# Optimization experiments

Hardware: AMD Instinct MI355X
Metric: run time of the kernel (lower is better)

The kernel has to match this reference:

```python
import jax, jax.numpy as jnp
import numpy as np

B, C, H, W = 8, 512, 96, 96
CQ = C // 4


def setup_inputs() -> dict:
    key = jax.random.key(0)
    ks = jax.random.split(key, 8)
    s = 1.0 / np.sqrt(C)
    return {
        "x": jax.random.normal(ks[0], (B, C, H, W), jnp.float32),
        "Wq": jax.random.normal(ks[1], (CQ, C), jnp.float32) * s,
        "bq": jax.random.normal(ks[2], (CQ,), jnp.float32) * 0.01,
        "Wk": jax.random.normal(ks[3], (CQ, C), jnp.float32) * s,
        "bk": jax.random.normal(ks[4], (CQ,), jnp.float32) * 0.01,
        "Wv": jax.random.normal(ks[5], (C, C), jnp.float32) * s,
        "bv": jax.random.normal(ks[6], (C,), jnp.float32) * 0.01,
        "gamma": jax.random.normal(ks[7], (1,), jnp.float32) * 0.1,
    }


def _conv1x1(x, Wt, b):
    # 1x1 conv == per-pixel channel matmul: [B,C,H,W] x [O,C] -> [B,O,H,W]
    return jnp.einsum("bchw,oc->bohw", x, Wt) + b[None, :, None, None]


def reference(x, Wq, bq, Wk, bk, Wv, bv, gamma):
    b, c, h, w = x.shape
    q = _conv1x1(x, Wq, bq)  # [B,CQ,H,W]
    k = _conv1x1(x, Wk, bk)  # [B,CQ,H,W]
    v = _conv1x1(x, Wv, bv)  # [B,C ,H,W]

    # column (height-axis) attention energies, diagonal masked to -inf
    energy_H = jnp.einsum("bchw,bcjw->bhwj", q, k)  # [B,H,W,H]
    diag = jnp.eye(h, dtype=bool)[:, None, :]  # [H,1,H] broadcast over W
    energy_H = jnp.where(diag[None], -jnp.inf, energy_H)
    # row (width-axis) attention energies
    energy_W = jnp.einsum("bchw,bchj->bhwj", q, k)  # [B,H,W,W]

    att = jax.nn.softmax(jnp.concatenate([energy_H, energy_W], axis=3), axis=3)
    att_H = att[..., :h]       # [B,H,W,H]
    att_W = att[..., h:h + w]  # [B,H,W,W]

    out_H = jnp.einsum("bcjw,bhwj->bchw", v, att_H)
    out_W = jnp.einsum("bchj,bhwj->bchw", v, att_W)
    return gamma[0] * (out_H + out_W) + x
```

## Files before the change

### kernel.cpp

```cpp
#include <hip/hip_runtime.h>


#define B_ 8
#define C_ 512
#define CQ_ 128
#define H_ 96
#define W_ 96
#define HW_ 9216
#define J_ 192

typedef __attribute__((ext_vector_type(8))) short short8;
typedef __attribute__((ext_vector_type(4))) float f32x4;

__device__ __forceinline__ unsigned short f2bf(float f) {
    unsigned u = __float_as_uint(f);
    u += 0x7FFFu + ((u >> 16) & 1u);
    return (unsigned short)(u >> 16);
}
__device__ __forceinline__ float bf2f(unsigned short h) {
    return __uint_as_float((unsigned)h << 16);
}
__device__ __forceinline__ unsigned short f2h(float f) {
    _Float16 h = (_Float16)f;
    return __builtin_bit_cast(unsigned short, h);
}
__device__ __forceinline__ float h2f(unsigned short u) {
    return (float)__builtin_bit_cast(_Float16, u);
}
__device__ __forceinline__ void gl_lds16(const unsigned short* g, void* lds_base) {
    __builtin_amdgcn_global_load_lds((const __attribute__((address_space(1))) void*)g,
                                     (__attribute__((address_space(3))) void*)lds_base,
                                     16, 0, 0);
}

__global__ __launch_bounds__(256) void k0_wconv(const float* __restrict__ Wq,
                                                const float* __restrict__ Wk,
                                                const float* __restrict__ Wv,
                                                unsigned short* __restrict__ Wqk,
                                                unsigned short* __restrict__ Wvb) {
    int i = blockIdx.x * 256 + threadIdx.x;
    if (i < 65536)        Wqk[i] = f2bf(Wq[i]);
    else if (i < 131072)  Wqk[i] = f2bf(Wk[i - 65536]);
    else                  Wvb[i - 131072] = f2bf(Wv[i - 131072]);
}

__global__ __launch_bounds__(256) void k1_xT(const float* __restrict__ x,
                                             unsigned short* __restrict__ xT) {
    __shared__ unsigned short t[32][33];
    int b = blockIdx.z, c0 = blockIdx.y * 32, p0 = blockIdx.x * 32;
    int tx = threadIdx.x, ty = threadIdx.y;
    const float* xb = x + (size_t)b * C_ * HW_;
    #pragma unroll
    for (int k = 0; k < 4; ++k) {
        int c = c0 + ty + k * 8;
        t[ty + k * 8][tx] = f2bf(xb[(size_t)c * HW_ + p0 + tx]);
    }
    __syncthreads();
    unsigned short* xTb = xT + (size_t)b * HW_ * C_;
    #pragma unroll
    for (int k = 0; k < 4; ++k) {
        int p = p0 + ty + k * 8;
        xTb[(size_t)p * C_ + c0 + tx] = t[tx][ty + k * 8];
    }
}

__global__ __launch_bounds__(512) void k2a_qk(const unsigned short* __restrict__ xT,
                                              const unsigned short* __restrict__ Wqk,
                                              const float* __restrict__ bq,
                                              const float* __restrict__ bk,
                                              unsigned short* __restrict__ Qb,
                                              unsigned short* __restrict__ Kb) {
    __shared__ alignas(16) unsigned short As[128][64];
    __shared__ alignas(16) unsigned short Bs[256][64];
    int t = threadIdx.x;
    int p0 = blockIdx.x * 128;
    int wid = t >> 6, lane = t & 63;
    int wr = wid >> 2, wc = wid & 3;
    int srow = lane >> 3, sk8 = (lane & 7) << 3;
    const f32x4 zero = {0.f, 0.f, 0.f, 0.f};
    f32x4 acc[4][4];
    for (int m = 0; m < 4; ++m) for (int n = 0; n < 4; ++n) acc[m][n] = zero;
    for (int ks = 0; ks < 512; ks += 64) {
        #pragma unroll
        for (int i = 0; i < 2; ++i) {
            int q = wid * 2 + i; int row = q * 8 + srow;
            gl_lds16(xT + ((size_t)(p0 + row) << 9) + ks + sk8, (char*)&As[0][0] + q * 1024);
        }
        #pragma unroll
        for (int i = 0; i < 4; ++i) {
            int q = wid * 4 + i; int row = q * 8 + srow;
            gl_lds16(Wqk + ((size_t)row << 9) + ks + sk8, (char*)&Bs[0][0] + q * 1024);
        }
        __syncthreads();
        #pragma unroll
        for (int kk = 0; kk < 2; ++kk) {
            int ko = (kk << 5) + ((lane >> 4) << 3);
            short8 af[4], bfv[4];
            #pragma unroll
            for (int m = 0; m < 4; ++m) af[m] = *(const short8*)(&As[wr * 64 + m * 16 + (lane & 15)][ko]);
            #pragma unroll
            for (int n = 0; n < 4; ++n) bfv[n] = *(const short8*)(&Bs[wc * 64 + n * 16 + (lane & 15)][ko]);
            #pragma unroll
            for (int m = 0; m < 4; ++m)
                #pragma unroll
                for (int n = 0; n < 4; ++n)
                    acc[m][n] = __builtin_amdgcn_mfma_f32_16x16x32_bf16(af[m], bfv[n], acc[m][n], 0, 0, 0);
        }
        __syncthreads();
    }
    #pragma unroll
    for (int n = 0; n < 4; ++n) {
        int oc = wc * 64 + n * 16 + (lane & 15);
        float bias = (oc < 128) ? bq[oc] : bk[oc - 128];
        unsigned short* dst = (oc < 128) ? (Qb + oc) : (Kb + (oc - 128));
        #pragma unroll
        for (int m = 0; m < 4; ++m) {
            int pr = p0 + wr * 64 + m * 16 + ((lane >> 4) << 2);
            #pragma unroll
            for (int r = 0; r < 4; ++r)
                dst[(size_t)(pr + r) << 7] = f2bf(acc[m][n][r] + bias);
        }
    }
}

__global__ __launch_bounds__(512) void k2b_v(const unsigned short* __restrict__ xT,
                                             const unsigned short* __restrict__ Wvb,
                                             const float* __restrict__ bv,
                                             unsigned short* __restrict__ Vn) {
    __shared__ alignas(16) unsigned short As[512][64];
    __shared__ alignas(16) unsigned short Bs[64][64];
    int t = threadIdx.x;
    int p0 = blockIdx.x * 64;
    int wid = t >> 6, lane = t & 63;
    int wr = wid >> 1, wc = wid & 1;
    int srow = lane >> 3, sk8 = (lane & 7) << 3;
    const f32x4 zero = {0.f, 0.f, 0.f, 0.f};
    f32x4 acc[8][2];
    for (int m = 0; m < 8; ++m) for (int n = 0; n < 2; ++n) acc[m][n] = zero;
    for (int ks = 0; ks < 512; ks += 64) {
        #pragma unroll
        for (int i = 0; i < 8; ++i) {
            int q = wid * 8 + i; int row = q * 8 + srow;
            gl_lds16(Wvb + ((size_t)row << 9) + ks + sk8, (char*)&As[0][0] + q * 1024);
        }
        {
            int q = wid; int row = q * 8 + srow;
            gl_lds16(xT + ((size_t)(p0 + row) << 9) + ks + sk8, (char*)&Bs[0][0] + q * 1024);
        }
        __syncthreads();
        #pragma unroll
        for (int kk = 0; kk < 2; ++kk) {
            int ko = (kk << 5) + ((lane >> 4) << 3);
            short8 af[8], bfv[2];
            #pragma unroll
            for (int m = 0; m < 8; ++m) af[m] = *(const short8*)(&As[wr * 128 + m * 16 + (lane & 15)][ko]);
            #pragma unroll
            for (int n = 0; n < 2; ++n) bfv[n] = *(const short8*)(&Bs[wc * 32 + n * 16 + (lane & 15)][ko]);
            #pragma unroll
            for (int m = 0; m < 8; ++m)
                #pragma unroll
                for (int n = 0; n < 2; ++n)
                    acc[m][n] = __builtin_amdgcn_mfma_f32_16x16x32_bf16(af[m], bfv[n], acc[m][n], 0, 0, 0);
        }
        __syncthreads();
    }
    int b = p0 / HW_;
    int hw0 = p0 - b * HW_;
    #pragma unroll
    for (int m = 0; m < 8; ++m) {
        int ocb = wr * 128 + m * 16 + ((lane >> 4) << 2);
        #pragma unroll
        for (int n = 0; n < 2; ++n) {
            int hw = hw0 + wc * 32 + n * 16 + (lane & 15);
            #pragma unroll
            for (int r = 0; r < 4; ++r) {
                int oc = ocb + r;
                Vn[(size_t)(b * C_ + oc) * HW_ + hw] = f2bf(acc[m][n][r] + bv[oc]);
            }
        }
    }
}

__global__ __launch_bounds__(256) void k3_vt(const unsigned short* __restrict__ Vn,
                                             unsigned short* __restrict__ Vt) {
    __shared__ unsigned short tl[96][97];
    int plane = blockIdx.x;
    const unsigned short* src = Vn + (size_t)plane * HW_;
    unsigned short* dst = Vt + (size_t)plane * HW_;
    for (int e = threadIdx.x; e < HW_; e += 256) tl[e / 96][e % 96] = src[e];
    __syncthreads();
    for (int e = threadIdx.x; e < HW_; e += 256) { int w = e / 96, h = e % 96; dst[e] = tl[h][w]; }
}

__global__ __launch_bounds__(256) void k4_energy(const unsigned short* __restrict__ Qb,
                                                 const unsigned short* __restrict__ Kb,
                                                 unsigned short* __restrict__ att) {
    __shared__ alignas(16) unsigned short Qs[96][136];
    __shared__ alignas(16) unsigned short Ks[96][136];
    int t = threadIdx.x;
    int modeH = blockIdx.z;
    int b = blockIdx.y, v0 = blockIdx.x;
    size_t base, rstride, obase_off, ostride;
    if (!modeH) {
        base      = (size_t)((b * H_ + v0) * W_) * CQ_;
        rstride   = CQ_;
        obase_off = (size_t)((b * H_ + v0) * W_) * J_ + H_;
        ostride   = J_;
    } else {
        base      = ((size_t)(b * H_) * W_ + v0) * CQ_;
        rstride   = (size_t)W_ * CQ_;
        obase_off = ((size_t)(b * H_) * W_ + v0) * J_;
        ostride   = (size_t)W_ * J_;
    }
    for (int q = t; q < 1536; q += 256) {
        int row = q >> 4, c8 = (q & 15) << 3;
        *(uint4*)(&Qs[row][c8]) = *(const uint4*)(Qb + base + (size_t)row * rstride + c8);
        *(uint4*)(&Ks[row][c8]) = *(const uint4*)(Kb + base + (size_t)row * rstride + c8);
    }
    __syncthreads();
    int wid = t >> 6, lane = t & 63;
    int wr = wid >> 1, wc = wid & 1;
    const f32x4 zero = {0.f, 0.f, 0.f, 0.f};
    f32x4 acc[3][3];
    for (int m = 0; m < 3; ++m) for (int n = 0; n < 3; ++n) acc[m][n] = zero;
    #pragma unroll
    for (int ks = 0; ks < 128; ks += 32) {
        int ko = ks + ((lane >> 4) << 3);
        short8 af[3], bfv[3];
        #pragma unroll
        for (int m = 0; m < 3; ++m) af[m] = *(const short8*)(&Qs[wr * 48 + m * 16 + (lane & 15)][ko]);
        #pragma unroll
        for (int n = 0; n < 3; ++n) bfv[n] = *(const short8*)(&Ks[wc * 48 + n * 16 + (lane & 15)][ko]);
        #pragma unroll
        for (int m = 0; m < 3; ++m)
            #pragma unroll
            for (int n = 0; n < 3; ++n)
                acc[m][n] = __builtin_amdgcn_mfma_f32_16x16x32_bf16(af[m], bfv[n], acc[m][n], 0, 0, 0);
    }
    unsigned short* ob = att + obase_off;
    #pragma unroll
    for (int m = 0; m < 3; ++m) {
        int i = wr * 48 + m * 16 + ((lane >> 4) << 2);
        #pragma unroll
        for (int n = 0; n < 3; ++n) {
            int j = wc * 48 + n * 16 + (lane & 15);
            #pragma unroll
            for (int r = 0; r < 4; ++r) {
                float v = acc[m][n][r];
                if (modeH && (i + r) == j) v = -__builtin_inff();
                ob[(size_t)(i + r) * ostride + j] = f2h(v);
            }
        }
    }
}

__global__ __launch_bounds__(256) void k5_softmax(const unsigned short* __restrict__ att,
                                                  unsigned short* __restrict__ att2) {
    int r = blockIdx.x * 4 + (threadIdx.x >> 6);
    int lane = threadIdx.x & 63;
    const unsigned short* row = att + (size_t)r * J_;
    float e0 = h2f(row[lane]), e1 = h2f(row[lane + 64]), e2 = h2f(row[lane + 128]);
    float m = fmaxf(e0, fmaxf(e1, e2));
    #pragma unroll
    for (int off = 32; off; off >>= 1) m = fmaxf(m, __shfl_xor(m, off, 64));
    float p0 = __expf(e0 - m), p1 = __expf(e1 - m), p2 = __expf(e2 - m);
    float s = p0 + p1 + p2;
    #pragma unroll
    for (int off = 32; off; off >>= 1) s += __shfl_xor(s, off, 64);
    float inv = 1.f / s;
    unsigned short* orow = att2 + (size_t)r * J_;
    orow[lane]       = f2bf(p0 * inv);
    orow[lane + 64]  = f2bf(p1 * inv);
    orow[lane + 128] = f2bf(p2 * inv);
}

template <int MODE>
__global__ __launch_bounds__(256) void k67_agg(const unsigned short* __restrict__ Vsrc,
                                               const unsigned short* __restrict__ att2,
                                               unsigned short* __restrict__ dst) {
    __shared__ alignas(16) unsigned short As[128][104];
    __shared__ alignas(16) unsigned short Bs[96][104];
    int t = threadIdx.x;
    int c0 = blockIdx.x * 128;
    int b = blockIdx.y / 96;
    int v0 = blockIdx.y % 96;
    size_t abase, bbase, bstride;
    if (MODE == 0) {
        abase = (size_t)(b * C_ + c0) * HW_ + (size_t)v0 * W_;
        bbase = (size_t)((b * H_ + v0) * W_) * J_ + H_;
        bstride = J_;
    } else {
        abase = ((size_t)(b * C_ + c0) * W_ + v0) * H_;
        bbase = ((size_t)(b * H_) * W_ + v0) * J_;
        bstride = (size_t)W_ * J_;
    }
    {
        int row = t >> 1, cs = (t & 1) * 6;
        const unsigned short* src = Vsrc + abase + (size_t)row * HW_;
        #pragma unroll
        for (int i = 0; i < 6; ++i)
            *(uint4*)(&As[row][(cs + i) * 8]) = *(const uint4*)(src + (cs + i) * 8);
    }
    if (t < 192) {
        int row = t >> 1, cs = (t & 1) * 6;
        const unsigned short* src = att2 + bbase + (size_t)row * bstride;
        #pragma unroll
        for (int i = 0; i < 6; ++i)
            *(uint4*)(&Bs[row][(cs + i) * 8]) = *(const uint4*)(src + (cs + i) * 8);
    }
    __syncthreads();
    int wid = t >> 6, lane = t & 63;
    const f32x4 zero = {0.f, 0.f, 0.f, 0.f};
    f32x4 acc[2][6];
    for (int m = 0; m < 2; ++m) for (int n = 0; n < 6; ++n) acc[m][n] = zero;
    #pragma unroll
    for (int ks = 0; ks < 96; ks += 32) {
        int ko = ks + ((lane >> 4) << 3);
        short8 af[2], bfv[6];
        #pragma unroll
        for (int m = 0; m < 2; ++m) af[m] = *(const short8*)(&As[wid * 32 + m * 16 + (lane & 15)][ko]);
        #pragma unroll
        for (int n = 0; n < 6; ++n) bfv[n] = *(const short8*)(&Bs[n * 16 + (lane & 15)][ko]);
        #pragma unroll
        for (int m = 0; m < 2; ++m)
            #pragma unroll
            for (int n = 0; n < 6; ++n)
                acc[m][n] = __builtin_amdgcn_mfma_f32_16x16x32_bf16(af[m], bfv[n], acc[m][n], 0, 0, 0);
    }
    #pragma unroll
    for (int m = 0; m < 2; ++m) {
        int crel = wid * 32 + m * 16 + ((lane >> 4) << 2);
        #pragma unroll
        for (int n = 0; n < 6; ++n) {
            int col = n * 16 + (lane & 15);
            #pragma unroll
            for (int r = 0; r < 4; ++r)
                dst[abase + (size_t)(crel + r) * HW_ + col] = f2bf(acc[m][n][r]);
        }
    }
}

__global__ __launch_bounds__(256) void k8b_combine(const unsigned short* __restrict__ tmpW,
                                                   const unsigned short* __restrict__ tmpHT,
                                                   const float* __restrict__ x,
                                                   const float* __restrict__ gamma_p,
                                                   float* __restrict__ outp) {
    __shared__ unsigned tlp[96][49];
    int plane = blockIdx.x;
    int t = threadIdx.x;
    const unsigned short* src = tmpHT + (size_t)plane * HW_;
    for (int e = t; e < 1152; e += 256) {
        int w = e / 12, h8 = (e % 12) * 8;
        uint4 v = *(const uint4*)(src + w * 96 + h8);
        tlp[w][(h8 >> 1) + 0] = v.x;
        tlp[w][(h8 >> 1) + 1] = v.y;
        tlp[w][(h8 >> 1) + 2] = v.z;
        tlp[w][(h8 >> 1) + 3] = v.w;
    }
    __syncthreads();
    float g = gamma_p[0];
    const unsigned short* wp = tmpW + (size_t)plane * HW_;
    const float* xp = x + (size_t)plane * HW_;
    float* op = outp + (size_t)plane * HW_;
    #pragma unroll
    for (int i = 0; i < 9; ++i) {
        int m = t + 256 * i;
        int h = m / 24, w0 = (m % 24) * 4;
        int off = h * 96 + w0;
        f32x4 xv = *(const f32x4*)(xp + off);
        uint2 tw = *(const uint2*)(wp + off);
        unsigned short ws0 = (unsigned short)(tw.x & 0xFFFF);
        unsigned short ws1 = (unsigned short)(tw.x >> 16);
        unsigned short ws2 = (unsigned short)(tw.y & 0xFFFF);
        unsigned short ws3 = (unsigned short)(tw.y >> 16);
        f32x4 o;
        #pragma unroll
        for (int r = 0; r < 4; ++r) {
            unsigned u = tlp[w0 + r][h >> 1];
            unsigned short hv = (h & 1) ? (unsigned short)(u >> 16) : (unsigned short)(u & 0xFFFF);
            unsigned short wv = (r == 0) ? ws0 : (r == 1) ? ws1 : (r == 2) ? ws2 : ws3;
            o[r] = g * (bf2f(wv) + bf2f(hv)) + xv[r];
        }
        *(f32x4*)(op + off) = o;
    }
}

extern "C" void kernel_launch(void* const* d_in, const int* in_sizes, int n_in,
                              void* d_out, int out_size, void* d_ws, size_t ws_size,
                              hipStream_t stream) {
    const float* x  = (const float*)d_in[0];
    const float* Wq = (const float*)d_in[1];
    const float* bq = (const float*)d_in[2];
    const float* Wk = (const float*)d_in[3];
    const float* bk = (const float*)d_in[4];
    const float* Wv = (const float*)d_in[5];
    const float* bv = (const float*)d_in[6];
    const float* gm = (const float*)d_in[7];
    float* out = (float*)d_out;
    char* ws = (char*)d_ws;

    unsigned short* xT    = (unsigned short*)(ws + 0);
    unsigned short* attf  = (unsigned short*)(ws + 0);
    unsigned short* Vt    = (unsigned short*)(ws + 0);
    unsigned short* Vn    = (unsigned short*)(ws + 75497472);
    unsigned short* Qb    = (unsigned short*)(ws + 150994944);
    unsigned short* Kb    = (unsigned short*)(ws + 169869312);
    unsigned short* att2  = (unsigned short*)(ws + 150994944);
    unsigned short* Wqk   = (unsigned short*)(ws + 188743680);
    unsigned short* Wvb   = (unsigned short*)(ws + 189005824);

    k0_wconv<<<1536, 256, 0, stream>>>(Wq, Wk, Wv, Wqk, Wvb);
    k1_xT<<<dim3(288, 16, 8), dim3(32, 8, 1), 0, stream>>>(x, xT);
    k2a_qk<<<576, 512, 0, stream>>>(xT, Wqk, bq, bk, Qb, Kb);
    k2b_v<<<1152, 512, 0, stream>>>(xT, Wvb, bv, Vn);
    k4_energy<<<dim3(96, 8, 2), 256, 0, stream>>>(Qb, Kb, attf);
    k5_softmax<<<18432, 256, 0, stream>>>(attf, att2);
    k3_vt<<<4096, 256, 0, stream>>>(Vn, Vt);
    k67_agg<0><<<dim3(4, 768), 256, 0, stream>>>(Vn, att2, Vn);
    k67_agg<1><<<dim3(4, 768), 256, 0, stream>>>(Vt, att2, Vt);
    k8b_combine<<<4096, 256, 0, stream>>>(Vn, Vt, x, gm, out);
}
```

Measured before the change: 379.0 us.

## Aggregate attention over x first, then apply the V projection with fused epilogue

Uses linearity of the 1x1 value conv to aggregate bf16 x with the attention weights first and apply Wv plus bias afterwards, since the attention rows sum to one. The projection GEMM's epilogue applies gamma and the residual directly, which removes the separate V GEMM output, the V transpose and the combine kernel. x is staged as bf16 planes and their transposes in the output buffer as scratch. The shared-memory tiles of the QK and projection GEMMs get an XOR swizzle to reduce bank conflicts. The risk is bf16 rounding of the summed aggregate across the two aggregation passes, and reuse of the output buffer as scratch.

```diff
diff --git a/kernel.cpp b/kernel.cpp
--- a/kernel.cpp
+++ b/kernel.cpp
@@ -45,7 +45,8 @@
 }
 
 __global__ __launch_bounds__(256) void k1_xT(const float* __restrict__ x,
-                                             unsigned short* __restrict__ xT) {
+                                             unsigned short* __restrict__ xT,
+                                             unsigned short* __restrict__ xP) {
     __shared__ unsigned short t[32][33];
     int b = blockIdx.z, c0 = blockIdx.y * 32, p0 = blockIdx.x * 32;
     int tx = threadIdx.x, ty = threadIdx.y;
@@ -53,7 +54,9 @@
     #pragma unroll
     for (int k = 0; k < 4; ++k) {
         int c = c0 + ty + k * 8;
-        t[ty + k * 8][tx] = f2bf(xb[(size_t)c * HW_ + p0 + tx]);
+        unsigned short v = f2bf(xb[(size_t)c * HW_ + p0 + tx]);
+        t[ty + k * 8][tx] = v;
+        xP[((size_t)b * C_ + c) * HW_ + p0 + tx] = v;
     }
     __syncthreads();
     unsigned short* xTb = xT + (size_t)b * HW_ * C_;
@@ -62,6 +65,17 @@
         int p = p0 + ty + k * 8;
         xTb[(size_t)p * C_ + c0 + tx] = t[tx][ty + k * 8];
     }
+}
+
+__global__ __launch_bounds__(256) void k3_vt(const unsigned short* __restrict__ src_,
+                                             unsigned short* __restrict__ dst_) {
+    __shared__ unsigned short tl[96][97];
+    int plane = blockIdx.x;
+    const unsigned short* src = src_ + (size_t)plane * HW_;
+    unsigned short* dst = dst_ + (size_t)plane * HW_;
+    for (int e = threadIdx.x; e < HW_; e += 256) tl[e / 96][e % 96] = src[e];
+    __syncthreads();
+    for (int e = threadIdx.x; e < HW_; e += 256) { int w = e / 96, h = e % 96; dst[e] = tl[h][w]; }
 }
 
 __global__ __launch_bounds__(512) void k2a_qk(const unsigned short* __restrict__ xT,
@@ -76,7 +90,8 @@
     int p0 = blockIdx.x * 128;
     int wid = t >> 6, lane = t & 63;
     int wr = wid >> 2, wc = wid & 3;
-    int srow = lane >> 3, sk8 = (lane & 7) << 3;
+    int srow = lane >> 3;
+    int sk8 = (((lane & 7) ^ srow) << 3);
     const f32x4 zero = {0.f, 0.f, 0.f, 0.f};
     f32x4 acc[4][4];
     for (int m = 0; m < 4; ++m) for (int n = 0; n < 4; ++n) acc[m][n] = zero;
@@ -94,12 +109,12 @@
         __syncthreads();
         #pragma unroll
         for (int kk = 0; kk < 2; ++kk) {
-            int ko = (kk << 5) + ((lane >> 4) << 3);
+            int po = (((kk * 4 + (lane >> 4)) ^ (lane & 7)) << 3);
             short8 af[4], bfv[4];
             #pragma unroll
-            for (int m = 0; m < 4; ++m) af[m] = *(const short8*)(&As[wr * 64 + m * 16 + (lane & 15)][ko]);
-            #pragma unroll
-            for (int n = 0; n < 4; ++n) bfv[n] = *(const short8*)(&Bs[wc * 64 + n * 16 + (lane & 15)][ko]);
+            for (int m = 0; m < 4; ++m) af[m] = *(const short8*)(&As[wr * 64 + m * 16 + (lane & 15)][po]);
+            #pragma unroll
+            for (int n = 0; n < 4; ++n) bfv[n] = *(const short8*)(&Bs[wc * 64 + n * 16 + (lane & 15)][po]);
             #pragma unroll
             for (int m = 0; m < 4; ++m)
                 #pragma unroll
@@ -121,75 +136,6 @@
                 dst[(size_t)(pr + r) << 7] = f2bf(acc[m][n][r] + bias);
         }
     }
-}
-
-__global__ __launch_bounds__(512) void k2b_v(const unsigned short* __restrict__ xT,
-                                             const unsigned short* __restrict__ Wvb,
-                                             const float* __restrict__ bv,
-                                             unsigned short* __restrict__ Vn) {
-    __shared__ alignas(16) unsigned short As[512][64];
-    __shared__ alignas(16) unsigned short Bs[64][64];
-    int t = threadIdx.x;
-    int p0 = blockIdx.x * 64;
-    int wid = t >> 6, lane = t & 63;
-    int wr = wid >> 1, wc = wid & 1;
-    int srow = lane >> 3, sk8 = (lane & 7) << 3;
-    const f32x4 zero = {0.f, 0.f, 0.f, 0.f};
-    f32x4 acc[8][2];
-    for (int m = 0; m < 8; ++m) for (int n = 0; n < 2; ++n) acc[m][n] = zero;
-    for (int ks = 0; ks < 512; ks += 64) {
-        #pragma unroll
-        for (int i = 0; i < 8; ++i) {
-            int q = wid * 8 + i; int row = q * 8 + srow;
-            gl_lds16(Wvb + ((size_t)row << 9) + ks + sk8, (char*)&As[0][0] + q * 1024);
-        }
-        {
-            int q = wid; int row = q * 8 + srow;
-            gl_lds16(xT + ((size_t)(p0 + row) << 9) + ks + sk8, (char*)&Bs[0][0] + q * 1024);
-        }
-        __syncthreads();
-        #pragma unroll
-        for (int kk = 0; kk < 2; ++kk) {
-            int ko = (kk << 5) + ((lane >> 4) << 3);
-            short8 af[8], bfv[2];
-            #pragma unroll
-            for (int m = 0; m < 8; ++m) af[m] = *(const short8*)(&As[wr * 128 + m * 16 + (lane & 15)][ko]);
-            #pragma unroll
-            for (int n = 0; n < 2; ++n) bfv[n] = *(const short8*)(&Bs[wc * 32 + n * 16 + (lane & 15)][ko]);
-            #pragma unroll
-            for (int m = 0; m < 8; ++m)
-                #pragma unroll
-                for (int n = 0; n < 2; ++n)
-                    acc[m][n] = __builtin_amdgcn_mfma_f32_16x16x32_bf16(af[m], bfv[n], acc[m][n], 0, 0, 0);
-        }
-        __syncthreads();
-    }
-    int b = p0 / HW_;
-    int hw0 = p0 - b * HW_;
-    #pragma unroll
-    for (int m = 0; m < 8; ++m) {
-        int ocb = wr * 128 + m * 16 + ((lane >> 4) << 2);
-        #pragma unroll
-        for (int n = 0; n < 2; ++n) {
-            int hw = hw0 + wc * 32 + n * 16 + (lane & 15);
-            #pragma unroll
-            for (int r = 0; r < 4; ++r) {
-                int oc = ocb + r;
-                Vn[(size_t)(b * C_ + oc) * HW_ + hw] = f2bf(acc[m][n][r] + bv[oc]);
-            }
-        }
-    }
-}
-
-__global__ __launch_bounds__(256) void k3_vt(const unsigned short* __restrict__ Vn,
-                                             unsigned short* __restrict__ Vt) {
-    __shared__ unsigned short tl[96][97];
-    int plane = blockIdx.x;
-    const unsigned short* src = Vn + (size_t)plane * HW_;
-    unsigned short* dst = Vt + (size_t)plane * HW_;
-    for (int e = threadIdx.x; e < HW_; e += 256) tl[e / 96][e % 96] = src[e];
-    __syncthreads();
-    for (int e = threadIdx.x; e < HW_; e += 256) { int w = e / 96, h = e % 96; dst[e] = tl[h][w]; }
 }
 
 __global__ __launch_bounds__(256) void k4_energy(const unsigned short* __restrict__ Qb,
@@ -275,113 +221,129 @@
 }
 
 template <int MODE>
-__global__ __launch_bounds__(256) void k67_agg(const unsigned short* __restrict__ Vsrc,
-                                               const unsigned short* __restrict__ att2,
-                                               unsigned short* __restrict__ dst) {
-    __shared__ alignas(16) unsigned short As[128][104];
-    __shared__ alignas(16) unsigned short Bs[96][104];
+__global__ __launch_bounds__(512) void k6_agg(const unsigned short* __restrict__ att2,
+                                              const unsigned short* __restrict__ Xsrc,
+                                              unsigned short* __restrict__ xAgg) {
+    __shared__ alignas(16) unsigned short As[96][104];
+    __shared__ alignas(16) unsigned short Bs[256][104];
     int t = threadIdx.x;
-    int c0 = blockIdx.x * 128;
+    int c0 = blockIdx.x * 256;
     int b = blockIdx.y / 96;
-    int v0 = blockIdx.y % 96;
-    size_t abase, bbase, bstride;
-    if (MODE == 0) {
-        abase = (size_t)(b * C_ + c0) * HW_ + (size_t)v0 * W_;
-        bbase = (size_t)((b * H_ + v0) * W_) * J_ + H_;
-        bstride = J_;
-    } else {
-        abase = ((size_t)(b * C_ + c0) * W_ + v0) * H_;
-        bbase = ((size_t)(b * H_) * W_ + v0) * J_;
-        bstride = (size_t)W_ * J_;
+    int v = blockIdx.y % 96;
+    size_t abase, astride;
+    if (MODE == 0) { abase = ((size_t)(b * HW_) + (size_t)v * 96) * J_ + 96; astride = J_; }
+    else           { abase = (size_t)(b * HW_) * J_ + (size_t)v * J_;        astride = (size_t)96 * J_; }
+    if (t < 192) {
+        int row = t >> 1, cs = (t & 1) * 6;
+        const unsigned short* src = att2 + abase + (size_t)row * astride;
+        #pragma unroll
+        for (int i = 0; i < 6; ++i)
+            *(uint4*)(&As[row][(cs + i) * 8]) = *(const uint4*)(src + (cs + i) * 8);
     }
     {
         int row = t >> 1, cs = (t & 1) * 6;
-        const unsigned short* src = Vsrc + abase + (size_t)row * HW_;
-        #pragma unroll
-        for (int i = 0; i < 6; ++i)
-            *(uint4*)(&As[row][(cs + i) * 8]) = *(const uint4*)(src + (cs + i) * 8);
-    }
-    if (t < 192) {
-        int row = t >> 1, cs = (t & 1) * 6;
-        const unsigned short* src = att2 + bbase + (size_t)row * bstride;
+        const unsigned short* src = Xsrc + ((size_t)(b * C_) + c0 + row) * HW_ + v * 96;
         #pragma unroll
         for (int i = 0; i < 6; ++i)
             *(uint4*)(&Bs[row][(cs + i) * 8]) = *(const uint4*)(src + (cs + i) * 8);
     }
     __syncthreads();
     int wid = t >> 6, lane = t & 63;
+    int wr = wid >> 2, wc = wid & 3;
     const f32x4 zero = {0.f, 0.f, 0.f, 0.f};
-    f32x4 acc[2][6];
-    for (int m = 0; m < 2; ++m) for (int n = 0; n < 6; ++n) acc[m][n] = zero;
+    f32x4 acc[3][4];
+    for (int m = 0; m < 3; ++m) for (int n = 0; n < 4; ++n) acc[m][n] = zero;
     #pragma unroll
     for (int ks = 0; ks < 96; ks += 32) {
         int ko = ks + ((lane >> 4) << 3);
-        short8 af[2], bfv[6];
-        #pragma unroll
-        for (int m = 0; m < 2; ++m) af[m] = *(const short8*)(&As[wid * 32 + m * 16 + (lane & 15)][ko]);
-        #pragma unroll
-        for (int n = 0; n < 6; ++n) bfv[n] = *(const short8*)(&Bs[n * 16 + (lane & 15)][ko]);
-        #pragma unroll
-        for (int m = 0; m < 2; ++m)
-            #pragma unroll
-            for (int n = 0; n < 6; ++n)
+        short8 af[3], bfv[4];
+        #pragma unroll
+        for (int m = 0; m < 3; ++m) af[m] = *(const short8*)(&As[wr * 48 + m * 16 + (lane & 15)][ko]);
+        #pragma unroll
+        for (int n = 0; n < 4; ++n) bfv[n] = *(const short8*)(&Bs[wc * 64 + n * 16 + (lane & 15)][ko]);
+        #pragma unroll
+        for (int m = 0; m < 3; ++m)
+            #pragma unroll
+            for (int n = 0; n < 4; ++n)
                 acc[m][n] = __builtin_amdgcn_mfma_f32_16x16x32_bf16(af[m], bfv[n], acc[m][n], 0, 0, 0);
     }
     #pragma unroll
-    for (int m = 0; m < 2; ++m) {
-        int crel = wid * 32 + m * 16 + ((lane >> 4) << 2);
-        #pragma unroll
-        for (int n = 0; n < 6; ++n) {
-            int col = n * 16 + (lane & 15);
-            #pragma unroll
-            for (int r = 0; r < 4; ++r)
-                dst[abase + (size_t)(crel + r) * HW_ + col] = f2bf(acc[m][n][r]);
-        }
-    }
-}
-
-__global__ __launch_bounds__(256) void k8b_combine(const unsigned short* __restrict__ tmpW,
-                                                   const unsigned short* __restrict__ tmpHT,
-                                                   const float* __restrict__ x,
-                                                   const float* __restrict__ gamma_p,
-                                                   float* __restrict__ outp) {
-    __shared__ unsigned tlp[96][49];
-    int plane = blockIdx.x;
+    for (int m = 0; m < 3; ++m) {
+        int orow = wr * 48 + m * 16 + ((lane >> 4) << 2);
+        #pragma unroll
+        for (int n = 0; n < 4; ++n) {
+            int c = c0 + wc * 64 + n * 16 + (lane & 15);
+            #pragma unroll
+            for (int r = 0; r < 4; ++r) {
+                int p = (MODE == 0) ? (v * 96 + orow + r) : ((orow + r) * 96 + v);
+                size_t o = ((size_t)(b * HW_) + p) * C_ + c;
+                if (MODE == 0) xAgg[o] = f2bf(acc[m][n][r]);
+                else           xAgg[o] = f2bf(bf2f(xAgg[o]) + acc[m][n][r]);
+            }
+        }
+    }
+}
+
+__global__ __launch_bounds__(512) void k9_proj(const unsigned short* __restrict__ xAgg,
+                                               const unsigned short* __restrict__ Wvb,
+                                               const float* __restrict__ bv,
+                                               const float* __restrict__ x,
+                                               const float* __restrict__ gamma_p,
+                                               float* __restrict__ outp) {
+    __shared__ alignas(16) unsigned short As[512][64];
+    __shared__ alignas(16) unsigned short Bs[64][64];
     int t = threadIdx.x;
-    const unsigned short* src = tmpHT + (size_t)plane * HW_;
-    for (int e = t; e < 1152; e += 256) {
-        int w = e / 12, h8 = (e % 12) * 8;
-        uint4 v = *(const uint4*)(src + w * 96 + h8);
-        tlp[w][(h8 >> 1) + 0] = v.x;
-        tlp[w][(h8 >> 1) + 1] = v.y;
-        tlp[w][(h8 >> 1) + 2] = v.z;
-        tlp[w][(h8 >> 1) + 3] = v.w;
-    }
-    __syncthreads();
+    int p0 = blockIdx.x * 64;
+    int wid = t >> 6, lane = t & 63;
+    int wr = wid >> 1, wc = wid & 1;
+    int srow = lane >> 3;
+    int sk8 = (((lane & 7) ^ srow) << 3);
+    const f32x4 zero = {0.f, 0.f, 0.f, 0.f};
+    f32x4 acc[8][2];
+    for (int m = 0; m < 8; ++m) for (int n = 0; n < 2; ++n) acc[m][n] = zero;
+    for (int ks = 0; ks < 512; ks += 64) {
+        #pragma unroll
+        for (int i = 0; i < 8; ++i) {
+            int q = wid * 8 + i; int row = q * 8 + srow;
+            gl_lds16(Wvb + ((size_t)row << 9) + ks + sk8, (char*)&As[0][0] + q * 1024);
+        }
+        {
+            int q = wid; int row = q * 8 + srow;
+            gl_lds16(xAgg + ((size_t)(p0 + row) << 9) + ks + sk8, (char*)&Bs[0][0] + q * 1024);
+        }
+        __syncthreads();
+        #pragma unroll
+        for (int kk = 0; kk < 2; ++kk) {
+            int po = (((kk * 4 + (lane >> 4)) ^ (lane & 7)) << 3);
+            short8 af[8], bfv[2];
+            #pragma unroll
+            for (int m = 0; m < 8; ++m) af[m] = *(const short8*)(&As[wr * 128 + m * 16 + (lane & 15)][po]);
+            #pragma unroll
+            for (int n = 0; n < 2; ++n) bfv[n] = *(const short8*)(&Bs[wc * 32 + n * 16 + (lane & 15)][po]);
+            #pragma unroll
+            for (int m = 0; m < 8; ++m)
+                #pragma unroll
+                for (int n = 0; n < 2; ++n)
+                    acc[m][n] = __builtin_amdgcn_mfma_f32_16x16x32_bf16(af[m], bfv[n], acc[m][n], 0, 0, 0);
+        }
+        __syncthreads();
+    }
+    int b = blockIdx.x / 144;
+    int hw0 = (blockIdx.x % 144) * 64;
     float g = gamma_p[0];
-    const unsigned short* wp = tmpW + (size_t)plane * HW_;
-    const float* xp = x + (size_t)plane * HW_;
-    float* op = outp + (size_t)plane * HW_;
-    #pragma unroll
-    for (int i = 0; i < 9; ++i) {
-        int m = t + 256 * i;
-        int h = m / 24, w0 = (m % 24) * 4;
-        int off = h * 96 + w0;
-        f32x4 xv = *(const f32x4*)(xp + off);
-        uint2 tw = *(const uint2*)(wp + off);
-        unsigned short ws0 = (unsigned short)(tw.x & 0xFFFF);
-        unsigned short ws1 = (unsigned short)(tw.x >> 16);
-        unsigned short ws2 = (unsigned short)(tw.y & 0xFFFF);
-        unsigned short ws3 = (unsigned short)(tw.y >> 16);
-        f32x4 o;
-        #pragma unroll
-        for (int r = 0; r < 4; ++r) {
-            unsigned u = tlp[w0 + r][h >> 1];
-            unsigned short hv = (h & 1) ? (unsigned short)(u >> 16) : (unsigned short)(u & 0xFFFF);
-            unsigned short wv = (r == 0) ? ws0 : (r == 1) ? ws1 : (r == 2) ? ws2 : ws3;
-            o[r] = g * (bf2f(wv) + bf2f(hv)) + xv[r];
-        }
-        *(f32x4*)(op + off) = o;
+    #pragma unroll
+    for (int m = 0; m < 8; ++m) {
+        int ocb = wr * 128 + m * 16 + ((lane >> 4) << 2);
+        #pragma unroll
+        for (int n = 0; n < 2; ++n) {
+            int hw = hw0 + wc * 32 + n * 16 + (lane & 15);
+            #pragma unroll
+            for (int r = 0; r < 4; ++r) {
+                int oc = ocb + r;
+                size_t o = ((size_t)(b * C_ + oc)) * HW_ + hw;
+                outp[o] = g * (acc[m][n][r] + bv[oc]) + x[o];
+            }
+        }
     }
 }
 
@@ -400,23 +362,23 @@
     char* ws = (char*)d_ws;
 
     unsigned short* xT    = (unsigned short*)(ws + 0);
-    unsigned short* attf  = (unsigned short*)(ws + 0);
-    unsigned short* Vt    = (unsigned short*)(ws + 0);
-    unsigned short* Vn    = (unsigned short*)(ws + 75497472);
-    unsigned short* Qb    = (unsigned short*)(ws + 150994944);
-    unsigned short* Kb    = (unsigned short*)(ws + 169869312);
-    unsigned short* att2  = (unsigned short*)(ws + 150994944);
-    unsigned short* Wqk   = (unsigned short*)(ws + 188743680);
-    unsigned short* Wvb   = (unsigned short*)(ws + 189005824);
+    unsigned short* xAgg  = (unsigned short*)(ws + 0);
+    unsigned short* Qb    = (unsigned short*)(ws + 75497472);
+    unsigned short* Kb    = (unsigned short*)(ws + 94371840);
+    unsigned short* attf  = (unsigned short*)(ws + 113246208);
+    unsigned short* att2  = (unsigned short*)(ws + 141557760);
+    unsigned short* Wqk   = (unsigned short*)(ws + 169869312);
+    unsigned short* Wvb   = (unsigned short*)(ws + 170131456);
+    unsigned short* xP    = (unsigned short*)d_out;
+    unsigned short* xPT   = xP + 37748736;
 
     k0_wconv<<<1536, 256, 0, stream>>>(Wq, Wk, Wv, Wqk, Wvb);
-    k1_xT<<<dim3(288, 16, 8), dim3(32, 8, 1), 0, stream>>>(x, xT);
+    k1_xT<<<dim3(288, 16, 8), dim3(32, 8, 1), 0, stream>>>(x, xT, xP);
     k2a_qk<<<576, 512, 0, stream>>>(xT, Wqk, bq, bk, Qb, Kb);
-    k2b_v<<<1152, 512, 0, stream>>>(xT, Wvb, bv, Vn);
+    k3_vt<<<4096, 256, 0, stream>>>(xP, xPT);
     k4_energy<<<dim3(96, 8, 2), 256, 0, stream>>>(Qb, Kb, attf);
     k5_softmax<<<18432, 256, 0, stream>>>(attf, att2);
-    k3_vt<<<4096, 256, 0, stream>>>(Vn, Vt);
-    k67_agg<0><<<dim3(4, 768), 256, 0, stream>>>(Vn, att2, Vn);
-    k67_agg<1><<<dim3(4, 768), 256, 0, stream>>>(Vt, att2, Vt);
-    k8b_combine<<<4096, 256, 0, stream>>>(Vn, Vt, x, gm, out);
-}
+    k6_agg<0><<<dim3(2, 768), 512, 0, stream>>>(att2, xP, xAgg);
+    k6_agg<1><<<dim3(2, 768), 512, 0, stream>>>(att2, xPT, xAgg);
+    k9_proj<<<1152, 512, 0, stream>>>(xAgg, Wvb, bv, x, gm, out);
+}
```

Measured after the change: 400.3 us. 1.06x slower.
